# Optimization experiments

Hardware: AMD Instinct MI355X
Metric: run time of the kernel (lower is better)

The kernel has to match this reference:

```python
import jax, jax.numpy as jnp
import numpy as np

N = 100000   # nodes
E = 640000   # edges (before self-loops)
G = 1000     # graphs in batch
D_IN = 100
D = 128
EPS = 1e-5


def setup_inputs() -> dict:
    key = jax.random.key(0)
    ks = jax.random.split(key, 12)
    x = jax.random.normal(ks[0], (N, D_IN), dtype=jnp.float32)
    edge_index = jax.random.randint(ks[1], (2, E), 0, N, dtype=jnp.int64)
    edge_weight = jax.random.uniform(ks[2], (E,), dtype=jnp.float32)
    batch = jnp.sort(jax.random.randint(ks[3], (N,), 0, G, dtype=jnp.int64))
    def glorot(k, shape):
        fan = shape[0]
        return jax.random.normal(k, shape, dtype=jnp.float32) / np.float32(np.sqrt(fan))
    return {
        "x": x, "edge_index": edge_index, "edge_weight": edge_weight, "batch": batch,
        "W0": glorot(ks[4], (D_IN, D)), "b0": jnp.zeros((D,), jnp.float32),
        "W1": glorot(ks[5], (D, D)),    "b1": jnp.zeros((D,), jnp.float32),
        "W2": glorot(ks[6], (D, D)),    "b2": jnp.zeros((D,), jnp.float32),
        "gamma": jnp.ones((3, D), jnp.float32), "beta": jnp.zeros((3, D), jnp.float32),
        "run_mean": jnp.zeros((3, D), jnp.float32), "run_var": jnp.ones((3, D), jnp.float32),
        "Wout": glorot(ks[7], (D, 1)), "bout": jnp.zeros((1,), jnp.float32),
    }


def reference(x, edge_index, edge_weight, batch, W0, b0, W1, b1, W2, b2,
              gamma, beta, run_mean, run_var, Wout, bout):
    n = x.shape[0]
    # add self-loops with weight 1 (GCNConv default)
    loop = jnp.arange(n, dtype=edge_index.dtype)
    src = jnp.concatenate([edge_index[0], loop])
    dst = jnp.concatenate([edge_index[1], loop])
    ew = jnp.concatenate([edge_weight, jnp.ones((n,), edge_weight.dtype)])
    # symmetric normalization: D^{-1/2} A D^{-1/2}
    deg = jax.ops.segment_sum(ew, dst, num_segments=n)
    dinv = jnp.where(deg > 0, jax.lax.rsqrt(deg), 0.0)
    norm = dinv[src] * ew * dinv[dst]            # [E+N]

    def gcn_bn_relu(h, W, b, g, bt, rm, rv):
        h = h @ W                                 # linear first (cheaper gather dim)
        agg = jax.ops.segment_sum(h[src] * norm[:, None], dst, num_segments=n)
        agg = agg + b
        # BatchNorm1d in eval mode (running stats); dropout is identity in eval
        agg = g * (agg - rm) * jax.lax.rsqrt(rv + EPS) + bt
        return jax.nn.relu(agg)

    h = gcn_bn_relu(x, W0, b0, gamma[0], beta[0], run_mean[0], run_var[0])
    h = gcn_bn_relu(h, W1, b1, gamma[1], beta[1], run_mean[1], run_var[1])
    h = gcn_bn_relu(h, W2, b2, gamma[2], beta[2], run_mean[2], run_var[2])

    # global mean pool over graphs
    counts = jax.ops.segment_sum(jnp.ones((n,), h.dtype), batch, num_segments=G)
    pooled = jax.ops.segment_sum(h, batch, num_segments=G) / jnp.maximum(counts, 1.0)[:, None]
    return pooled @ Wout + bout
```

## Files before the change

### kernel.cpp

```cpp
#include <hip/hip_runtime.h>

#define BN_EPS 1e-5f
#define BINCAP 32

static inline size_t align_up(size_t x, size_t a) { return (x + a - 1) & ~(a - 1); }

typedef __attribute__((ext_vector_type(8))) short bf16x8;
typedef __attribute__((ext_vector_type(4))) float f32x4;

__device__ __forceinline__ void bf16split(float v, unsigned short& hi, unsigned short& lo) {
    unsigned u = __float_as_uint(v);
    unsigned rh = (u + 0x7FFFu + ((u >> 16) & 1u)) >> 16;
    float fh = __uint_as_float(rh << 16);
    hi = (unsigned short)rh;
    float rem = v - fh;
    unsigned u2 = __float_as_uint(rem);
    lo = (unsigned short)((u2 + 0x7FFFu + ((u2 >> 16) & 1u)) >> 16);
}

__device__ __forceinline__ unsigned short bf16rne(float v) {
    unsigned u = __float_as_uint(v);
    return (unsigned short)((u + 0x7FFFu + ((u >> 16) & 1u)) >> 16);
}

__device__ __forceinline__ float bf16f(unsigned h) { return __uint_as_float(h << 16); }
__device__ __forceinline__ float chlo(unsigned u) { return __uint_as_float(u << 16); }
__device__ __forceinline__ float chhi(unsigned u) { return __uint_as_float(u & 0xffff0000u); }


__global__ void place_kernel(const int* __restrict__ src, const int* __restrict__ dst,
                             const float* __restrict__ ew,
                             int* __restrict__ cntc, int2* __restrict__ bins, int E) {
    int e = blockIdx.x * blockDim.x + threadIdx.x;
    if (e >= E) return;
    int d = dst[e];
    int pos = atomicAdd(&cntc[d], 1);
    if (pos < BINCAP)
        bins[(size_t)d * BINCAP + pos] = make_int2(src[e], __float_as_int(ew[e]));
}


__global__ void deginv_kernel(const int* __restrict__ cntc, const int2* __restrict__ bins,
                              float* __restrict__ dinv, int N) {
    int i = blockIdx.x * blockDim.x + threadIdx.x;
    if (i >= N) return;
    int cnt = cntc[i]; if (cnt > BINCAP) cnt = BINCAP;
    const int2* b = bins + (size_t)i * BINCAP;
    float s = 0.f;
    for (int j = 0; j < cnt; ++j) s += __int_as_float(b[j].y);
    dinv[i] = rsqrtf(s + 1.0f);
}


__global__ void normfix_kernel(const int* __restrict__ cntc, int2* __restrict__ bins,
                               const float* __restrict__ dinv, int N) {
    int i = blockIdx.x * blockDim.x + threadIdx.x;
    if (i >= N) return;
    int cnt = cntc[i]; if (cnt > BINCAP) cnt = BINCAP;
    float di = dinv[i];
    int2* b = bins + (size_t)i * BINCAP;
    for (int j = 0; j < cnt; ++j) {
        int2 pr = b[j];
        float w = __int_as_float(pr.y) * dinv[pr.x] * di;
        b[j].y = __float_as_int(w);
    }
}


__global__ void convw_kernel(const float* __restrict__ W0, const float* __restrict__ W1,
                             const float* __restrict__ W2, int K0,
                             unsigned short* __restrict__ Whi, unsigned short* __restrict__ Wlo) {
    int idx = blockIdx.x * blockDim.x + threadIdx.x;
    if (idx >= 3 * 32 * 64 * 8) return;
    int j    = idx & 7;
    int lane = (idx >> 3) & 63;
    int f    = (idx >> 9) & 31;
    int l    = idx >> 14;
    int ct = f >> 2, k0c = f & 3;
    int quad = lane >> 4, m16 = lane & 15;
    int n = ct * 16 + m16;
    int k = k0c * 32 + quad * 8 + j;
    const float* W = (l == 0) ? W0 : (l == 1) ? W1 : W2;
    int Kl = (l == 0) ? K0 : 128;
    float v = (k < Kl) ? W[(size_t)k * 128 + n] : 0.f;
    unsigned short hi, lo;
    bf16split(v, hi, lo);
    Whi[idx] = hi;
    Wlo[idx] = lo;
}


__global__ void convx_kernel(const float* __restrict__ x, int D_IN,
                             unsigned int* __restrict__ Phi, unsigned int* __restrict__ Plo,
                             int N) {
    int idx = blockIdx.x * blockDim.x + threadIdx.x;
    int node = idx >> 6, h = idx & 63;
    if (node >= N) return;
    int k = h * 2;
    float a = (k     < D_IN) ? x[(size_t)node * D_IN + k]     : 0.f;
    float b = (k + 1 < D_IN) ? x[(size_t)node * D_IN + k + 1] : 0.f;
    unsigned short ha, la, hb, lb;
    bf16split(a, ha, la);
    bf16split(b, hb, lb);
    Phi[(size_t)node * 64 + h] = (unsigned)ha | ((unsigned)hb << 16);
    Plo[(size_t)node * 64 + h] = (unsigned)la | ((unsigned)lb << 16);
}


__device__ __forceinline__ void mfma_tail(const bf16x8 ah[4], const bf16x8 al[4],
                                          const unsigned short* __restrict__ Whi,
                                          const unsigned short* __restrict__ Wlo,
                                          unsigned short* __restrict__ Yh,
                                          int row0, int quad, int m16, int lane, int N) {
    const bf16x8* Wh8 = (const bf16x8*)Whi;
    const bf16x8* Wl8 = (const bf16x8*)Wlo;

    f32x4 acc[8];
    #pragma unroll
    for (int ct = 0; ct < 8; ++ct) acc[ct] = (f32x4){0.f, 0.f, 0.f, 0.f};

    bf16x8 bh[2][4], bl[2][4];
    #pragma unroll
    for (int k0c = 0; k0c < 4; ++k0c) {
        bh[0][k0c] = Wh8[k0c * 64 + lane];
        bl[0][k0c] = Wl8[k0c * 64 + lane];
    }

    #pragma unroll
    for (int ct = 0; ct < 8; ++ct) {
        int cur = ct & 1, nxt = cur ^ 1;
        if (ct < 7) {
            #pragma unroll
            for (int k0c = 0; k0c < 4; ++k0c) {
                bh[nxt][k0c] = Wh8[((ct + 1) * 4 + k0c) * 64 + lane];
                bl[nxt][k0c] = Wl8[((ct + 1) * 4 + k0c) * 64 + lane];
            }
        }
        #pragma unroll
        for (int k0c = 0; k0c < 4; ++k0c) {
            acc[ct] = __builtin_amdgcn_mfma_f32_16x16x32_bf16(ah[k0c], bh[cur][k0c], acc[ct], 0, 0, 0);
            acc[ct] = __builtin_amdgcn_mfma_f32_16x16x32_bf16(ah[k0c], bl[cur][k0c], acc[ct], 0, 0, 0);
            acc[ct] = __builtin_amdgcn_mfma_f32_16x16x32_bf16(al[k0c], bh[cur][k0c], acc[ct], 0, 0, 0);
        }
    }

    #pragma unroll
    for (int ct = 0; ct < 8; ++ct) {
        #pragma unroll
        for (int rg = 0; rg < 4; ++rg) {
            int row = row0 + quad * 4 + rg;
            if (row < N)
                Yh[(size_t)row * 128 + ct * 16 + m16] = bf16rne(acc[ct][rg]);
        }
    }
}


__launch_bounds__(256, 2)
__global__ void gemm_mfma_kernel(const unsigned short* __restrict__ Phi,
                                 const unsigned short* __restrict__ Plo,
                                 const unsigned short* __restrict__ Whi,
                                 const unsigned short* __restrict__ Wlo,
                                 unsigned short* __restrict__ Yh, int N) {
    int tid = threadIdx.x;
    int wid = tid >> 6, lane = tid & 63;
    int quad = lane >> 4, m16 = lane & 15;
    int row0 = blockIdx.x * 64 + wid * 16;

    int arow = row0 + m16;
    if (arow > N - 1) arow = N - 1;
    const unsigned short* phi = Phi + (size_t)arow * 128 + quad * 8;
    const unsigned short* plo = Plo + (size_t)arow * 128 + quad * 8;

    bf16x8 ah[4], al[4];
    #pragma unroll
    for (int k0c = 0; k0c < 4; ++k0c) {
        ah[k0c] = *(const bf16x8*)(phi + k0c * 32);
        al[k0c] = *(const bf16x8*)(plo + k0c * 32);
    }

    mfma_tail(ah, al, Whi, Wlo, Yh, row0, quad, m16, lane, N);
}


__global__ void scaleshift_kernel(const float* __restrict__ gamma, const float* __restrict__ beta,
                                  const float* __restrict__ rm, const float* __restrict__ rv,
                                  const float* __restrict__ b0, const float* __restrict__ b1,
                                  const float* __restrict__ b2,
                                  float* __restrict__ scale, float* __restrict__ shift) {
    int t = threadIdx.x;
    int l = t >> 7, j = t & 127;
    const float* bs = (l == 0) ? b0 : (l == 1) ? b1 : b2;
    float sc = gamma[t] * rsqrtf(rv[t] + BN_EPS);
    scale[t] = sc;
    shift[t] = beta[t] + (bs[j] - rm[t]) * sc;
}


__device__ __forceinline__ void gather_bin(const unsigned* __restrict__ Yh32,
                                           const int2* __restrict__ bin, int m,
                                           int node, int lane,
                                           float& ax, float& ay) {
    int2 pr = (lane < m) ? bin[lane] : make_int2(node, 0);
    int mr = (m + 7) & ~7;
    for (int j = 0; j < mr; j += 8) {
        int   s0 = __builtin_amdgcn_readlane(pr.x, j);
        int   s1 = __builtin_amdgcn_readlane(pr.x, j + 1);
        int   s2 = __builtin_amdgcn_readlane(pr.x, j + 2);
        int   s3 = __builtin_amdgcn_readlane(pr.x, j + 3);
        int   s4 = __builtin_amdgcn_readlane(pr.x, j + 4);
        int   s5 = __builtin_amdgcn_readlane(pr.x, j + 5);
        int   s6 = __builtin_amdgcn_readlane(pr.x, j + 6);
        int   s7 = __builtin_amdgcn_readlane(pr.x, j + 7);
        float w0e = __int_as_float(__builtin_amdgcn_readlane(pr.y, j));
        float w1e = __int_as_float(__builtin_amdgcn_readlane(pr.y, j + 1));
        float w2e = __int_as_float(__builtin_amdgcn_readlane(pr.y, j + 2));
        float w3e = __int_as_float(__builtin_amdgcn_readlane(pr.y, j + 3));
        float w4e = __int_as_float(__builtin_amdgcn_readlane(pr.y, j + 4));
        float w5e = __int_as_float(__builtin_amdgcn_readlane(pr.y, j + 5));
        float w6e = __int_as_float(__builtin_amdgcn_readlane(pr.y, j + 6));
        float w7e = __int_as_float(__builtin_amdgcn_readlane(pr.y, j + 7));
        unsigned u0 = Yh32[(size_t)s0 * 64 + lane];
        unsigned u1 = Yh32[(size_t)s1 * 64 + lane];
        unsigned u2 = Yh32[(size_t)s2 * 64 + lane];
        unsigned u3 = Yh32[(size_t)s3 * 64 + lane];
        unsigned u4 = Yh32[(size_t)s4 * 64 + lane];
        unsigned u5 = Yh32[(size_t)s5 * 64 + lane];
        unsigned u6 = Yh32[(size_t)s6 * 64 + lane];
        unsigned u7 = Yh32[(size_t)s7 * 64 + lane];
        ax += chlo(u0) * w0e; ay += chhi(u0) * w0e;
        ax += chlo(u1) * w1e; ay += chhi(u1) * w1e;
        ax += chlo(u2) * w2e; ay += chhi(u2) * w2e;
        ax += chlo(u3) * w3e; ay += chhi(u3) * w3e;
        ax += chlo(u4) * w4e; ay += chhi(u4) * w4e;
        ax += chlo(u5) * w5e; ay += chhi(u5) * w5e;
        ax += chlo(u6) * w6e; ay += chhi(u6) * w6e;
        ax += chlo(u7) * w7e; ay += chhi(u7) * w7e;
    }
}


__device__ __forceinline__ void gather_bin2(const unsigned* __restrict__ Yh32,
                                            const int2* __restrict__ bin0, int m0, int node0,
                                            const int2* __restrict__ bin1, int m1, int node1,
                                            int lane,
                                            float& ax0, float& ay0, float& ax1, float& ay1) {
    int2 pr0 = (lane < m0) ? bin0[lane] : make_int2(node0, 0);
    int2 pr1 = (lane < m1) ? bin1[lane] : make_int2(node1, 0);
    int mr0 = (m0 + 7) & ~7, mr1 = (m1 + 7) & ~7;
    int mr = mr0 > mr1 ? mr0 : mr1;
    for (int j = 0; j < mr; j += 8) {
        int a0 = __builtin_amdgcn_readlane(pr0.x, j);
        int a1 = __builtin_amdgcn_readlane(pr0.x, j + 1);
        int a2 = __builtin_amdgcn_readlane(pr0.x, j + 2);
        int a3 = __builtin_amdgcn_readlane(pr0.x, j + 3);
        int a4 = __builtin_amdgcn_readlane(pr0.x, j + 4);
        int a5 = __builtin_amdgcn_readlane(pr0.x, j + 5);
        int a6 = __builtin_amdgcn_readlane(pr0.x, j + 6);
        int a7 = __builtin_amdgcn_readlane(pr0.x, j + 7);
        int b0 = __builtin_amdgcn_readlane(pr1.x, j);
        int b1 = __builtin_amdgcn_readlane(pr1.x, j + 1);
        int b2 = __builtin_amdgcn_readlane(pr1.x, j + 2);
        int b3 = __builtin_amdgcn_readlane(pr1.x, j + 3);
        int b4 = __builtin_amdgcn_readlane(pr1.x, j + 4);
        int b5 = __builtin_amdgcn_readlane(pr1.x, j + 5);
        int b6 = __builtin_amdgcn_readlane(pr1.x, j + 6);
        int b7 = __builtin_amdgcn_readlane(pr1.x, j + 7);
        float wa0 = __int_as_float(__builtin_amdgcn_readlane(pr0.y, j));
        float wa1 = __int_as_float(__builtin_amdgcn_readlane(pr0.y, j + 1));
        float wa2 = __int_as_float(__builtin_amdgcn_readlane(pr0.y, j + 2));
        float wa3 = __int_as_float(__builtin_amdgcn_readlane(pr0.y, j + 3));
        float wa4 = __int_as_float(__builtin_amdgcn_readlane(pr0.y, j + 4));
        float wa5 = __int_as_float(__builtin_amdgcn_readlane(pr0.y, j + 5));
        float wa6 = __int_as_float(__builtin_amdgcn_readlane(pr0.y, j + 6));
        float wa7 = __int_as_float(__builtin_amdgcn_readlane(pr0.y, j + 7));
        float wb0 = __int_as_float(__builtin_amdgcn_readlane(pr1.y, j));
        float wb1 = __int_as_float(__builtin_amdgcn_readlane(pr1.y, j + 1));
        float wb2 = __int_as_float(__builtin_amdgcn_readlane(pr1.y, j + 2));
        float wb3 = __int_as_float(__builtin_amdgcn_readlane(pr1.y, j + 3));
        float wb4 = __int_as_float(__builtin_amdgcn_readlane(pr1.y, j + 4));
        float wb5 = __int_as_float(__builtin_amdgcn_readlane(pr1.y, j + 5));
        float wb6 = __int_as_float(__builtin_amdgcn_readlane(pr1.y, j + 6));
        float wb7 = __int_as_float(__builtin_amdgcn_readlane(pr1.y, j + 7));
        unsigned ua0 = Yh32[(size_t)a0 * 64 + lane];
        unsigned ua1 = Yh32[(size_t)a1 * 64 + lane];
        unsigned ua2 = Yh32[(size_t)a2 * 64 + lane];
        unsigned ua3 = Yh32[(size_t)a3 * 64 + lane];
        unsigned ua4 = Yh32[(size_t)a4 * 64 + lane];
        unsigned ua5 = Yh32[(size_t)a5 * 64 + lane];
        unsigned ua6 = Yh32[(size_t)a6 * 64 + lane];
        unsigned ua7 = Yh32[(size_t)a7 * 64 + lane];
        unsigned ub0 = Yh32[(size_t)b0 * 64 + lane];
        unsigned ub1 = Yh32[(size_t)b1 * 64 + lane];
        unsigned ub2 = Yh32[(size_t)b2 * 64 + lane];
        unsigned ub3 = Yh32[(size_t)b3 * 64 + lane];
        unsigned ub4 = Yh32[(size_t)b4 * 64 + lane];
        unsigned ub5 = Yh32[(size_t)b5 * 64 + lane];
        unsigned ub6 = Yh32[(size_t)b6 * 64 + lane];
        unsigned ub7 = Yh32[(size_t)b7 * 64 + lane];
        ax0 += chlo(ua0) * wa0; ay0 += chhi(ua0) * wa0;
        ax0 += chlo(ua1) * wa1; ay0 += chhi(ua1) * wa1;
        ax0 += chlo(ua2) * wa2; ay0 += chhi(ua2) * wa2;
        ax0 += chlo(ua3) * wa3; ay0 += chhi(ua3) * wa3;
        ax0 += chlo(ua4) * wa4; ay0 += chhi(ua4) * wa4;
        ax0 += chlo(ua5) * wa5; ay0 += chhi(ua5) * wa5;
        ax0 += chlo(ua6) * wa6; ay0 += chhi(ua6) * wa6;
        ax0 += chlo(ua7) * wa7; ay0 += chhi(ua7) * wa7;
        ax1 += chlo(ub0) * wb0; ay1 += chhi(ub0) * wb0;
        ax1 += chlo(ub1) * wb1; ay1 += chhi(ub1) * wb1;
        ax1 += chlo(ub2) * wb2; ay1 += chhi(ub2) * wb2;
        ax1 += chlo(ub3) * wb3; ay1 += chhi(ub3) * wb3;
        ax1 += chlo(ub4) * wb4; ay1 += chhi(ub4) * wb4;
        ax1 += chlo(ub5) * wb5; ay1 += chhi(ub5) * wb5;
        ax1 += chlo(ub6) * wb6; ay1 += chhi(ub6) * wb6;
        ax1 += chlo(ub7) * wb7; ay1 += chhi(ub7) * wb7;
    }
}


__launch_bounds__(256, 2)
__global__ void fused_agg_gemm_kernel(
        const unsigned* __restrict__ Yh_in,
        const int2* __restrict__ bins, const int* __restrict__ cntc,
        const float* __restrict__ dinv,
        const float* __restrict__ scale, const float* __restrict__ shift,
        const unsigned short* __restrict__ Whi, const unsigned short* __restrict__ Wlo,
        unsigned short* __restrict__ Yh_out, int N) {
    __shared__ float sA[4][16 * 132];
    int tid = threadIdx.x;
    int wid = tid >> 6, lane = tid & 63;
    int quad = lane >> 4, m16 = lane & 15;
    int row0 = blockIdx.x * 64 + wid * 16;
    float* my = sA[wid];

    float2 sc = ((const float2*)scale)[lane];
    float2 sh = ((const float2*)shift)[lane];

    for (int i = 0; i < 16; i += 2) {
        int n0 = row0 + i;     if (n0 > N - 1) n0 = N - 1;
        int n1 = row0 + i + 1; if (n1 > N - 1) n1 = N - 1;
        float d0 = dinv[n0], d1 = dinv[n1];
        float w00 = d0 * d0, w01 = d1 * d1;
        unsigned uh0 = Yh_in[(size_t)n0 * 64 + lane];
        unsigned uh1 = Yh_in[(size_t)n1 * 64 + lane];
        float ax0 = chlo(uh0) * w00, ay0 = chhi(uh0) * w00;
        float ax1 = chlo(uh1) * w01, ay1 = chhi(uh1) * w01;
        int m0 = cntc[n0]; if (m0 > BINCAP) m0 = BINCAP;
        int m1 = cntc[n1]; if (m1 > BINCAP) m1 = BINCAP;
        gather_bin2(Yh_in, bins + (size_t)n0 * BINCAP, m0, n0,
                    bins + (size_t)n1 * BINCAP, m1, n1, lane,
                    ax0, ay0, ax1, ay1);
        float ox0 = fmaxf(ax0 * sc.x + sh.x, 0.f);
        float oy0 = fmaxf(ay0 * sc.y + sh.y, 0.f);
        float ox1 = fmaxf(ax1 * sc.x + sh.x, 0.f);
        float oy1 = fmaxf(ay1 * sc.y + sh.y, 0.f);
        *((float2*)&my[i * 132 + 2 * lane])       = make_float2(ox0, oy0);
        *((float2*)&my[(i + 1) * 132 + 2 * lane]) = make_float2(ox1, oy1);
    }
    __syncthreads();

    bf16x8 ah[4], al[4];
    #pragma unroll
    for (int k0c = 0; k0c < 4; ++k0c) {
        float4 v0 = *((const float4*)&my[m16 * 132 + k0c * 32 + quad * 8]);
        float4 v1 = *((const float4*)&my[m16 * 132 + k0c * 32 + quad * 8 + 4]);
        float vs[8] = {v0.x, v0.y, v0.z, v0.w, v1.x, v1.y, v1.z, v1.w};
        #pragma unroll
        for (int j = 0; j < 8; ++j) {
            unsigned short hi, lo;
            bf16split(vs[j], hi, lo);
            ah[k0c][j] = (short)hi;
            al[k0c][j] = (short)lo;
        }
    }

    mfma_tail(ah, al, Whi, Wlo, Yh_out, row0, quad, m16, lane, N);
}


__launch_bounds__(256)
__global__ void agg3_kernel(const unsigned* __restrict__ Yh32,
                            const int2* __restrict__ bins, const int* __restrict__ cntc,
                            const float* __restrict__ dinv,
                            const float* __restrict__ scale, const float* __restrict__ shift,
                            const float* __restrict__ Wout,
                            float* __restrict__ snode, int N) {
    int idx = blockIdx.x * blockDim.x + threadIdx.x;
    int node = idx >> 6, lane = idx & 63;
    if (node >= N) return;

    float d = dinv[node];
    float w0 = d * d;
    unsigned uh = Yh32[(size_t)node * 64 + lane];
    float ax = chlo(uh) * w0;
    float ay = chhi(uh) * w0;

    int m = cntc[node]; if (m > BINCAP) m = BINCAP;
    gather_bin(Yh32, bins + (size_t)node * BINCAP, m, node, lane, ax, ay);

    float2 sc = ((const float2*)scale)[lane];
    float2 sh = ((const float2*)shift)[lane];
    float ox = fmaxf(ax * sc.x + sh.x, 0.f);
    float oy = fmaxf(ay * sc.y + sh.y, 0.f);
    float2 w = ((const float2*)Wout)[lane];
    float s = ox * w.x + oy * w.y;
    #pragma unroll
    for (int off = 32; off > 0; off >>= 1) s += __shfl_down(s, off, 64);
    if (lane == 0) snode[node] = s;
}


__global__ void bounds_kernel(const int* __restrict__ batch, int* __restrict__ gstart,
                              int N, int G) {
    int i = blockIdx.x * blockDim.x + threadIdx.x;
    if (i >= N) return;
    int b = batch[i];
    int prev = (i == 0) ? -1 : batch[i - 1];
    for (int g = prev + 1; g <= b; ++g) gstart[g] = i;
    if (i == N - 1) {
        for (int g = b + 1; g <= G; ++g) gstart[g] = N;
    }
}

__launch_bounds__(256)
__global__ void pool3_kernel(const float* __restrict__ snode, const int* __restrict__ gstart,
                             const float* __restrict__ bout, float* __restrict__ out, int G) {
    int g = blockIdx.x;
    int beg = gstart[g], end = gstart[g + 1];
    int t = threadIdx.x;
    float acc = 0.f;
    for (int n = beg + t; n < end; n += 256) acc += snode[n];
    __shared__ float lds[256];
    lds[t] = acc;
    __syncthreads();
    if (t < 64) lds[t] = lds[t] + lds[t + 64] + lds[t + 128] + lds[t + 192];
    __syncthreads();
    if (t < 64) {
        float s = lds[t];
        #pragma unroll
        for (int off = 32; off > 0; off >>= 1) s += __shfl_down(s, off, 64);
        if (t == 0) {
            float cntf = (float)(end - beg);
            out[g] = s / fmaxf(cntf, 1.0f) + bout[0];
        }
    }
}


extern "C" void kernel_launch(void* const* d_in, const int* in_sizes, int n_in,
                              void* d_out, int out_size, void* d_ws, size_t ws_size,
                              hipStream_t stream) {
    const float* x     = (const float*)d_in[0];
    const int*   ei    = (const int*)d_in[1];
    const float* ew    = (const float*)d_in[2];
    const int*   batch = (const int*)d_in[3];
    const float* W0 = (const float*)d_in[4];
    const float* b0 = (const float*)d_in[5];
    const float* W1 = (const float*)d_in[6];
    const float* b1 = (const float*)d_in[7];
    const float* W2 = (const float*)d_in[8];
    const float* b2 = (const float*)d_in[9];
    const float* gamma = (const float*)d_in[10];
    const float* beta  = (const float*)d_in[11];
    const float* rmean = (const float*)d_in[12];
    const float* rvar  = (const float*)d_in[13];
    const float* Wout  = (const float*)d_in[14];
    const float* bout  = (const float*)d_in[15];

    const int E = in_sizes[2];
    const int N = in_sizes[3];
    const int D_IN = in_sizes[0] / N;
    const int G = out_size;

    const int* src = ei;
    const int* dst = ei + E;

    char* ws = (char*)d_ws;
    size_t off = 0;
    float* dinv  = (float*)(ws + off); off = align_up(off + (size_t)N * 4, 256);
    int* cntc    = (int*)(ws + off);   off = align_up(off + (size_t)N * 4, 256);
    int* gstart  = (int*)(ws + off);   off = align_up(off + ((size_t)G + 1) * 4, 256);
    int2* bins   = (int2*)(ws + off);  off = align_up(off + (size_t)N * BINCAP * 8, 256);
    unsigned short* YAh = (unsigned short*)(ws + off); off = align_up(off + (size_t)N * 128 * 2, 256);
    unsigned short* YBh = (unsigned short*)(ws + off); off = align_up(off + (size_t)N * 128 * 2, 256);
    unsigned short* Phi = (unsigned short*)(ws + off); off = align_up(off + (size_t)N * 128 * 2, 256);
    unsigned short* Plo = (unsigned short*)(ws + off); off = align_up(off + (size_t)N * 128 * 2, 256);
    unsigned short* Whi = (unsigned short*)(ws + off); off = align_up(off + 3 * 16384 * 2, 256);
    unsigned short* Wlo = (unsigned short*)(ws + off); off = align_up(off + 3 * 16384 * 2, 256);
    float* scale = (float*)(ws + off); off = align_up(off + 3 * 128 * 4, 256);
    float* shift = (float*)(ws + off); off = align_up(off + 3 * 128 * 4, 256);
    float* snode = (float*)(ws + off); off = align_up(off + (size_t)N * 4, 256);
    (void)ws_size;

    hipMemsetAsync(cntc, 0, (size_t)N * 4, stream);

    const int tB = 256;
    place_kernel<<<(E + tB - 1) / tB, tB, 0, stream>>>(src, dst, ew, cntc, bins, E);
    deginv_kernel<<<(N + tB - 1) / tB, tB, 0, stream>>>(cntc, bins, dinv, N);
    normfix_kernel<<<(N + tB - 1) / tB, tB, 0, stream>>>(cntc, bins, dinv, N);
    bounds_kernel<<<(N + tB - 1) / tB, tB, 0, stream>>>(batch, gstart, N, G);
    scaleshift_kernel<<<1, 384, 0, stream>>>(gamma, beta, rmean, rvar, b0, b1, b2, scale, shift);
    convw_kernel<<<(3 * 32 * 64 * 8 + tB - 1) / tB, tB, 0, stream>>>(W0, W1, W2, D_IN, Whi, Wlo);
    {
        long nt = (long)N * 64;
        convx_kernel<<<(int)((nt + tB - 1) / tB), tB, 0, stream>>>(x, D_IN,
            (unsigned int*)Phi, (unsigned int*)Plo, N);
    }

    long nthread_node = (long)N * 64;
    int blocks_node = (int)((nthread_node + tB - 1) / tB);
    int gemm_blocks = (N + 63) / 64;

    gemm_mfma_kernel<<<gemm_blocks, 256, 0, stream>>>(Phi, Plo, Whi, Wlo, YAh, N);
    fused_agg_gemm_kernel<<<gemm_blocks, 256, 0, stream>>>(
        (const unsigned*)YAh, bins, cntc, dinv,
        scale, shift, Whi + 16384, Wlo + 16384, YBh, N);
    fused_agg_gemm_kernel<<<gemm_blocks, 256, 0, stream>>>(
        (const unsigned*)YBh, bins, cntc, dinv,
        scale + 128, shift + 128, Whi + 2 * 16384, Wlo + 2 * 16384, YAh, N);
    agg3_kernel<<<blocks_node, tB, 0, stream>>>((const unsigned*)YAh,
        bins, cntc, dinv, scale + 256, shift + 256, Wout, snode, N);

    pool3_kernel<<<G, 256, 0, stream>>>(snode, gstart, bout, (float*)d_out, G);
}
```

Baseline: 357.1 us.

## Fuse x conversion into first GEMM, prefetch bin metadata, pair nodes in agg3

Removes the separate convx pass and its hi/lo bf16 staging buffers. The first GEMM now loads fp32 x directly with float4 reads and splits it into bf16 hi/lo in registers. The fused agg+GEMM kernel prefetches counts, dinv, self features and bin entries for all 16 rows up front. It also replaces the block barrier with an LDS waitcnt plus sched_barrier, which assumes each wave reads only the rows it wrote itself. The MFMA loop is wrapped in s_setprio, and agg3 now processes two nodes per wave to overlap gathers. The gain comes from less memory traffic, one fewer launch and more memory-level parallelism, at the cost of higher register pressure.

After: 340.3 us. 4.7% less time.

```diff
diff --git a/kernel.cpp b/kernel.cpp
--- a/kernel.cpp
+++ b/kernel.cpp
@@ -90,23 +90,6 @@
 }
 
 
-__global__ void convx_kernel(const float* __restrict__ x, int D_IN,
-                             unsigned int* __restrict__ Phi, unsigned int* __restrict__ Plo,
-                             int N) {
-    int idx = blockIdx.x * blockDim.x + threadIdx.x;
-    int node = idx >> 6, h = idx & 63;
-    if (node >= N) return;
-    int k = h * 2;
-    float a = (k     < D_IN) ? x[(size_t)node * D_IN + k]     : 0.f;
-    float b = (k + 1 < D_IN) ? x[(size_t)node * D_IN + k + 1] : 0.f;
-    unsigned short ha, la, hb, lb;
-    bf16split(a, ha, la);
-    bf16split(b, hb, lb);
-    Phi[(size_t)node * 64 + h] = (unsigned)ha | ((unsigned)hb << 16);
-    Plo[(size_t)node * 64 + h] = (unsigned)la | ((unsigned)lb << 16);
-}
-
-
 __device__ __forceinline__ void mfma_tail(const bf16x8 ah[4], const bf16x8 al[4],
                                           const unsigned short* __restrict__ Whi,
                                           const unsigned short* __restrict__ Wlo,
@@ -126,6 +109,7 @@
         bl[0][k0c] = Wl8[k0c * 64 + lane];
     }
 
+    __builtin_amdgcn_s_setprio(1);
     #pragma unroll
     for (int ct = 0; ct < 8; ++ct) {
         int cur = ct & 1, nxt = cur ^ 1;
@@ -143,6 +127,7 @@
             acc[ct] = __builtin_amdgcn_mfma_f32_16x16x32_bf16(al[k0c], bh[cur][k0c], acc[ct], 0, 0, 0);
         }
     }
+    __builtin_amdgcn_s_setprio(0);
 
     #pragma unroll
     for (int ct = 0; ct < 8; ++ct) {
@@ -157,11 +142,10 @@
 
 
 __launch_bounds__(256, 2)
-__global__ void gemm_mfma_kernel(const unsigned short* __restrict__ Phi,
-                                 const unsigned short* __restrict__ Plo,
-                                 const unsigned short* __restrict__ Whi,
-                                 const unsigned short* __restrict__ Wlo,
-                                 unsigned short* __restrict__ Yh, int N) {
+__global__ void gemm0_fused_kernel(const float* __restrict__ x, int D_IN,
+                                   const unsigned short* __restrict__ Whi,
+                                   const unsigned short* __restrict__ Wlo,
+                                   unsigned short* __restrict__ Yh, int N) {
     int tid = threadIdx.x;
     int wid = tid >> 6, lane = tid & 63;
     int quad = lane >> 4, m16 = lane & 15;
@@ -169,14 +153,29 @@
 
     int arow = row0 + m16;
     if (arow > N - 1) arow = N - 1;
-    const unsigned short* phi = Phi + (size_t)arow * 128 + quad * 8;
-    const unsigned short* plo = Plo + (size_t)arow * 128 + quad * 8;
+    const float* xr = x + (size_t)arow * D_IN;
 
     bf16x8 ah[4], al[4];
     #pragma unroll
     for (int k0c = 0; k0c < 4; ++k0c) {
-        ah[k0c] = *(const bf16x8*)(phi + k0c * 32);
-        al[k0c] = *(const bf16x8*)(plo + k0c * 32);
+        int kb = k0c * 32 + quad * 8;
+        float vs[8];
+        if (kb + 8 <= D_IN) {
+            float4 v0 = *((const float4*)(xr + kb));
+            float4 v1 = *((const float4*)(xr + kb + 4));
+            vs[0] = v0.x; vs[1] = v0.y; vs[2] = v0.z; vs[3] = v0.w;
+            vs[4] = v1.x; vs[5] = v1.y; vs[6] = v1.z; vs[7] = v1.w;
+        } else {
+            #pragma unroll
+            for (int j = 0; j < 8; ++j) vs[j] = (kb + j < D_IN) ? xr[kb + j] : 0.f;
+        }
+        #pragma unroll
+        for (int j = 0; j < 8; ++j) {
+            unsigned short hi, lo;
+            bf16split(vs[j], hi, lo);
+            ah[k0c][j] = (short)hi;
+            al[k0c][j] = (short)lo;
+        }
     }
 
     mfma_tail(ah, al, Whi, Wlo, Yh, row0, quad, m16, lane, N);
@@ -197,56 +196,10 @@
 }
 
 
-__device__ __forceinline__ void gather_bin(const unsigned* __restrict__ Yh32,
-                                           const int2* __restrict__ bin, int m,
-                                           int node, int lane,
-                                           float& ax, float& ay) {
-    int2 pr = (lane < m) ? bin[lane] : make_int2(node, 0);
-    int mr = (m + 7) & ~7;
-    for (int j = 0; j < mr; j += 8) {
-        int   s0 = __builtin_amdgcn_readlane(pr.x, j);
-        int   s1 = __builtin_amdgcn_readlane(pr.x, j + 1);
-        int   s2 = __builtin_amdgcn_readlane(pr.x, j + 2);
-        int   s3 = __builtin_amdgcn_readlane(pr.x, j + 3);
-        int   s4 = __builtin_amdgcn_readlane(pr.x, j + 4);
-        int   s5 = __builtin_amdgcn_readlane(pr.x, j + 5);
-        int   s6 = __builtin_amdgcn_readlane(pr.x, j + 6);
-        int   s7 = __builtin_amdgcn_readlane(pr.x, j + 7);
-        float w0e = __int_as_float(__builtin_amdgcn_readlane(pr.y, j));
-        float w1e = __int_as_float(__builtin_amdgcn_readlane(pr.y, j + 1));
-        float w2e = __int_as_float(__builtin_amdgcn_readlane(pr.y, j + 2));
-        float w3e = __int_as_float(__builtin_amdgcn_readlane(pr.y, j + 3));
-        float w4e = __int_as_float(__builtin_amdgcn_readlane(pr.y, j + 4));
-        float w5e = __int_as_float(__builtin_amdgcn_readlane(pr.y, j + 5));
-        float w6e = __int_as_float(__builtin_amdgcn_readlane(pr.y, j + 6));
-        float w7e = __int_as_float(__builtin_amdgcn_readlane(pr.y, j + 7));
-        unsigned u0 = Yh32[(size_t)s0 * 64 + lane];
-        unsigned u1 = Yh32[(size_t)s1 * 64 + lane];
-        unsigned u2 = Yh32[(size_t)s2 * 64 + lane];
-        unsigned u3 = Yh32[(size_t)s3 * 64 + lane];
-        unsigned u4 = Yh32[(size_t)s4 * 64 + lane];
-        unsigned u5 = Yh32[(size_t)s5 * 64 + lane];
-        unsigned u6 = Yh32[(size_t)s6 * 64 + lane];
-        unsigned u7 = Yh32[(size_t)s7 * 64 + lane];
-        ax += chlo(u0) * w0e; ay += chhi(u0) * w0e;
-        ax += chlo(u1) * w1e; ay += chhi(u1) * w1e;
-        ax += chlo(u2) * w2e; ay += chhi(u2) * w2e;
-        ax += chlo(u3) * w3e; ay += chhi(u3) * w3e;
-        ax += chlo(u4) * w4e; ay += chhi(u4) * w4e;
-        ax += chlo(u5) * w5e; ay += chhi(u5) * w5e;
-        ax += chlo(u6) * w6e; ay += chhi(u6) * w6e;
-        ax += chlo(u7) * w7e; ay += chhi(u7) * w7e;
-    }
-}
-
-
-__device__ __forceinline__ void gather_bin2(const unsigned* __restrict__ Yh32,
-                                            const int2* __restrict__ bin0, int m0, int node0,
-                                            const int2* __restrict__ bin1, int m1, int node1,
+__device__ __forceinline__ void gather_pair(const unsigned* __restrict__ Yh32,
+                                            int2 pr0, int m0, int2 pr1, int m1,
                                             int lane,
                                             float& ax0, float& ay0, float& ax1, float& ay1) {
-    int2 pr0 = (lane < m0) ? bin0[lane] : make_int2(node0, 0);
-    int2 pr1 = (lane < m1) ? bin1[lane] : make_int2(node1, 0);
     int mr0 = (m0 + 7) & ~7, mr1 = (m1 + 7) & ~7;
     int mr = mr0 > mr1 ? mr0 : mr1;
     for (int j = 0; j < mr; j += 8) {
@@ -336,20 +289,28 @@
     float2 sc = ((const float2*)scale)[lane];
     float2 sh = ((const float2*)shift)[lane];
 
+    int mm[16]; float dv[16]; unsigned uh[16]; int2 gg[16];
+    #pragma unroll
+    for (int i = 0; i < 16; ++i) {
+        int n = row0 + i; if (n > N - 1) n = N - 1;
+        mm[i] = cntc[n];
+        dv[i] = dinv[n];
+        uh[i] = Yh_in[(size_t)n * 64 + lane];
+        gg[i] = bins[(size_t)n * BINCAP + (lane & 31)];
+    }
+
+    #pragma unroll
     for (int i = 0; i < 16; i += 2) {
         int n0 = row0 + i;     if (n0 > N - 1) n0 = N - 1;
         int n1 = row0 + i + 1; if (n1 > N - 1) n1 = N - 1;
-        float d0 = dinv[n0], d1 = dinv[n1];
-        float w00 = d0 * d0, w01 = d1 * d1;
-        unsigned uh0 = Yh_in[(size_t)n0 * 64 + lane];
-        unsigned uh1 = Yh_in[(size_t)n1 * 64 + lane];
-        float ax0 = chlo(uh0) * w00, ay0 = chhi(uh0) * w00;
-        float ax1 = chlo(uh1) * w01, ay1 = chhi(uh1) * w01;
-        int m0 = cntc[n0]; if (m0 > BINCAP) m0 = BINCAP;
-        int m1 = cntc[n1]; if (m1 > BINCAP) m1 = BINCAP;
-        gather_bin2(Yh_in, bins + (size_t)n0 * BINCAP, m0, n0,
-                    bins + (size_t)n1 * BINCAP, m1, n1, lane,
-                    ax0, ay0, ax1, ay1);
+        int m0 = mm[i];     if (m0 > BINCAP) m0 = BINCAP;
+        int m1 = mm[i + 1]; if (m1 > BINCAP) m1 = BINCAP;
+        float w00 = dv[i] * dv[i], w01 = dv[i + 1] * dv[i + 1];
+        float ax0 = chlo(uh[i]) * w00,     ay0 = chhi(uh[i]) * w00;
+        float ax1 = chlo(uh[i + 1]) * w01, ay1 = chhi(uh[i + 1]) * w01;
+        int2 pr0 = (lane < m0) ? gg[i]     : make_int2(n0, 0);
+        int2 pr1 = (lane < m1) ? gg[i + 1] : make_int2(n1, 0);
+        gather_pair(Yh_in, pr0, m0, pr1, m1, lane, ax0, ay0, ax1, ay1);
         float ox0 = fmaxf(ax0 * sc.x + sh.x, 0.f);
         float oy0 = fmaxf(ay0 * sc.y + sh.y, 0.f);
         float ox1 = fmaxf(ax1 * sc.x + sh.x, 0.f);
@@ -357,7 +318,9 @@
         *((float2*)&my[i * 132 + 2 * lane])       = make_float2(ox0, oy0);
         *((float2*)&my[(i + 1) * 132 + 2 * lane]) = make_float2(ox1, oy1);
     }
-    __syncthreads();
+
+    asm volatile("s_waitcnt lgkmcnt(0)" ::: "memory");
+    __builtin_amdgcn_sched_barrier(0);
 
     bf16x8 ah[4], al[4];
     #pragma unroll
@@ -386,27 +349,46 @@
                             const float* __restrict__ Wout,
                             float* __restrict__ snode, int N) {
     int idx = blockIdx.x * blockDim.x + threadIdx.x;
-    int node = idx >> 6, lane = idx & 63;
-    if (node >= N) return;
-
-    float d = dinv[node];
-    float w0 = d * d;
-    unsigned uh = Yh32[(size_t)node * 64 + lane];
-    float ax = chlo(uh) * w0;
-    float ay = chhi(uh) * w0;
-
-    int m = cntc[node]; if (m > BINCAP) m = BINCAP;
-    gather_bin(Yh32, bins + (size_t)node * BINCAP, m, node, lane, ax, ay);
+    int pairid = idx >> 6, lane = idx & 63;
+    int n0 = pairid * 2;
+    if (n0 >= N) return;
+    int n1 = n0 + 1; if (n1 > N - 1) n1 = n0;
+
+    int m0 = cntc[n0];
+    int m1 = cntc[n1];
+    float d0 = dinv[n0], d1 = dinv[n1];
+    unsigned uh0 = Yh32[(size_t)n0 * 64 + lane];
+    unsigned uh1 = Yh32[(size_t)n1 * 64 + lane];
+    int2 g0 = bins[(size_t)n0 * BINCAP + (lane & 31)];
+    int2 g1 = bins[(size_t)n1 * BINCAP + (lane & 31)];
+    if (m0 > BINCAP) m0 = BINCAP;
+    if (m1 > BINCAP) m1 = BINCAP;
+
+    float w00 = d0 * d0, w01 = d1 * d1;
+    float ax0 = chlo(uh0) * w00, ay0 = chhi(uh0) * w00;
+    float ax1 = chlo(uh1) * w01, ay1 = chhi(uh1) * w01;
+    int2 pr0 = (lane < m0) ? g0 : make_int2(n0, 0);
+    int2 pr1 = (lane < m1) ? g1 : make_int2(n1, 0);
+    gather_pair(Yh32, pr0, m0, pr1, m1, lane, ax0, ay0, ax1, ay1);
 
     float2 sc = ((const float2*)scale)[lane];
     float2 sh = ((const float2*)shift)[lane];
-    float ox = fmaxf(ax * sc.x + sh.x, 0.f);
-    float oy = fmaxf(ay * sc.y + sh.y, 0.f);
-    float2 w = ((const float2*)Wout)[lane];
-    float s = ox * w.x + oy * w.y;
-    #pragma unroll
-    for (int off = 32; off > 0; off >>= 1) s += __shfl_down(s, off, 64);
-    if (lane == 0) snode[node] = s;
+    float2 w  = ((const float2*)Wout)[lane];
+    float ox0 = fmaxf(ax0 * sc.x + sh.x, 0.f);
+    float oy0 = fmaxf(ay0 * sc.y + sh.y, 0.f);
+    float ox1 = fmaxf(ax1 * sc.x + sh.x, 0.f);
+    float oy1 = fmaxf(ay1 * sc.y + sh.y, 0.f);
+    float s0 = ox0 * w.x + oy0 * w.y;
+    float s1 = ox1 * w.x + oy1 * w.y;
+    #pragma unroll
+    for (int off = 32; off > 0; off >>= 1) {
+        s0 += __shfl_down(s0, off, 64);
+        s1 += __shfl_down(s1, off, 64);
+    }
+    if (lane == 0) {
+        snode[n0] = s0;
+        if (n1 != n0) snode[n1] = s1;
+    }
 }
 
 
@@ -483,8 +465,6 @@
     int2* bins   = (int2*)(ws + off);  off = align_up(off + (size_t)N * BINCAP * 8, 256);
     unsigned short* YAh = (unsigned short*)(ws + off); off = align_up(off + (size_t)N * 128 * 2, 256);
     unsigned short* YBh = (unsigned short*)(ws + off); off = align_up(off + (size_t)N * 128 * 2, 256);
-    unsigned short* Phi = (unsigned short*)(ws + off); off = align_up(off + (size_t)N * 128 * 2, 256);
-    unsigned short* Plo = (unsigned short*)(ws + off); off = align_up(off + (size_t)N * 128 * 2, 256);
     unsigned short* Whi = (unsigned short*)(ws + off); off = align_up(off + 3 * 16384 * 2, 256);
     unsigned short* Wlo = (unsigned short*)(ws + off); off = align_up(off + 3 * 16384 * 2, 256);
     float* scale = (float*)(ws + off); off = align_up(off + 3 * 128 * 4, 256);
@@ -501,25 +481,22 @@
     bounds_kernel<<<(N + tB - 1) / tB, tB, 0, stream>>>(batch, gstart, N, G);
     scaleshift_kernel<<<1, 384, 0, stream>>>(gamma, beta, rmean, rvar, b0, b1, b2, scale, shift);
     convw_kernel<<<(3 * 32 * 64 * 8 + tB - 1) / tB, tB, 0, stream>>>(W0, W1, W2, D_IN, Whi, Wlo);
-    {
-        long nt = (long)N * 64;
-        convx_kernel<<<(int)((nt + tB - 1) / tB), tB, 0, stream>>>(x, D_IN,
-            (unsigned int*)Phi, (unsigned int*)Plo, N);
-    }
-
-    long nthread_node = (long)N * 64;
-    int blocks_node = (int)((nthread_node + tB - 1) / tB);
+
     int gemm_blocks = (N + 63) / 64;
 
-    gemm_mfma_kernel<<<gemm_blocks, 256, 0, stream>>>(Phi, Plo, Whi, Wlo, YAh, N);
+    gemm0_fused_kernel<<<gemm_blocks, 256, 0, stream>>>(x, D_IN, Whi, Wlo, YAh, N);
     fused_agg_gemm_kernel<<<gemm_blocks, 256, 0, stream>>>(
         (const unsigned*)YAh, bins, cntc, dinv,
         scale, shift, Whi + 16384, Wlo + 16384, YBh, N);
     fused_agg_gemm_kernel<<<gemm_blocks, 256, 0, stream>>>(
         (const unsigned*)YBh, bins, cntc, dinv,
         scale + 128, shift + 128, Whi + 2 * 16384, Wlo + 2 * 16384, YAh, N);
-    agg3_kernel<<<blocks_node, tB, 0, stream>>>((const unsigned*)YAh,
-        bins, cntc, dinv, scale + 256, shift + 256, Wout, snode, N);
+    {
+        long nthread_pair = (long)((N + 1) / 2) * 64;
+        int blocks_pair = (int)((nthread_pair + tB - 1) / tB);
+        agg3_kernel<<<blocks_pair, tB, 0, stream>>>((const unsigned*)YAh,
+            bins, cntc, dinv, scale + 256, shift + 256, Wout, snode, N);
+    }
 
     pool3_kernel<<<G, 256, 0, stream>>>(snode, gstart, bout, (float*)d_out, G);
 }
```
